# Performance work log

Measured on AMD Instinct MI355X. Metric: run time of the kernel, lower is better.

Reference implementation:

```python
import jax, jax.numpy as jnp
import numpy as np

PARTS_NUM = 16
MAX_INIT = -100.0  # torch scatter_reduce amax include_self initial value


def setup_inputs() -> dict:
    key = jax.random.key(0)
    k1, k2 = jax.random.split(key)
    x = jax.random.normal(k1, (32, 256, 30, 16, 16), dtype=jnp.float32)
    part_labels = jax.random.randint(k2, (32, 30, 16, 16), 0, PARTS_NUM, dtype=jnp.int64)
    return {"x": x, "part_labels": part_labels}


def reference(x, part_labels):
    n, c, s, h, w = x.shape
    ns = n * s
    hw = h * w
    P = PARTS_NUM
    # feat: (ns*hw, c) -- channels-last for efficient segment reductions
    feat = jnp.transpose(x, (0, 2, 3, 4, 1)).reshape(ns * hw, c)
    labels = part_labels.reshape(ns, hw).astype(jnp.int32)
    # one flat segment id per (frame, part) pair
    seg = (labels + jnp.arange(ns, dtype=jnp.int32)[:, None] * P).reshape(ns * hw)
    num_seg = ns * P
    pooled_sum = jax.ops.segment_sum(feat, seg, num_segments=num_seg)          # (ns*P, c)
    pooled_count = jax.ops.segment_sum(jnp.ones((ns * hw,), feat.dtype), seg,
                                       num_segments=num_seg)                   # (ns*P,)
    pooled_max = jax.ops.segment_max(feat, seg, num_segments=num_seg)          # (ns*P, c)
    valid = (pooled_count > 0)[:, None]                                        # (ns*P, 1)
    pooled_mean = pooled_sum / jnp.maximum(pooled_count, 1.0)[:, None]
    # torch scatter_reduce includes initial -100.0 in the amax; empty parts -> 0
    pooled_max = jnp.where(valid, jnp.maximum(pooled_max, MAX_INIT), 0.0)
    pooled = pooled_mean + pooled_max                                          # (ns*P, c)
    # -> (n, c, s, P)
    return jnp.transpose(pooled.reshape(n, s, P, c), (0, 3, 1, 2))
```

## Files before the change

kernel.cpp:

```cpp
#include <hip/hip_runtime.h>


#define C_DIM 256
#define S_DIM 30
#define P_NUM 16
#define HW 256
#define CH_PER_BLK 64
#define TILE_STRIDE 260

__global__ __launch_bounds__(256, 2)
void partpp_pool_kernel(const float* __restrict__ x,
                        const int* __restrict__ labels,
                        float* __restrict__ out) {
    __shared__ float tile[CH_PER_BLK * TILE_STRIDE];
    __shared__ int pos_sorted[HW];
    __shared__ int counts[P_NUM];
    __shared__ int cursor[P_NUM];
    __shared__ int offs[P_NUM + 1];

    const int t  = threadIdx.x;
    const int b  = blockIdx.x;
    const int f  = b >> 2;
    const int q  = b & 3;
    const int ch0 = q * CH_PER_BLK;
    const int n  = f / S_DIM;
    const int s  = f - n * S_DIM;

    if (t < P_NUM) { counts[t] = 0; cursor[t] = 0; }
    __syncthreads();
    const int lab = labels[f * HW + t];
    atomicAdd(&counts[lab], 1);
    __syncthreads();
    if (t == 0) {
        int acc = 0;
        #pragma unroll
        for (int p = 0; p < P_NUM; ++p) { offs[p] = acc; acc += counts[p]; }
        offs[P_NUM] = acc;
    }
    __syncthreads();
    {
        const int r = atomicAdd(&cursor[lab], 1);
        pos_sorted[offs[lab] + r] = t;
    }
    __syncthreads();

    const size_t xbase = ((size_t)(n * C_DIM + ch0) * S_DIM + s) * HW;
    #pragma unroll
    for (int j = 0; j < 16; ++j) {
        const int flat = j * 256 + t;
        const int row  = flat >> 6;
        const int col  = flat & 63;
        const float4 v = *(const float4*)(x + xbase + (size_t)row * (S_DIM * HW) + col * 4);
        *(float4*)(&tile[row * TILE_STRIDE + col * 4]) = v;
    }
    __syncthreads();

    const int ch_l = t >> 2;
    const int sub  = t & 3;
    const float* rowp = &tile[ch_l * TILE_STRIDE];

    float res[4];
    #pragma unroll
    for (int pi = 0; pi < 4; ++pi) {
        const int p  = sub * 4 + pi;
        const int jb = offs[p];
        const int je = offs[p + 1];
        float sum = 0.0f;
        float mx  = -3.0e38f;
        for (int j = jb; j < je; ++j) {
            const float v = rowp[pos_sorted[j]];
            sum += v;
            mx = fmaxf(mx, v);
        }
        const int cnt = je - jb;
        res[pi] = (cnt > 0) ? (sum / (float)cnt + fmaxf(mx, -100.0f)) : 0.0f;
    }

    float* op = out + ((size_t)(n * C_DIM + ch0 + ch_l) * S_DIM + s) * P_NUM + sub * 4;
    *(float4*)op = make_float4(res[0], res[1], res[2], res[3]);
}

extern "C" void kernel_launch(void* const* d_in, const int* in_sizes, int n_in,
                              void* d_out, int out_size, void* d_ws, size_t ws_size,
                              hipStream_t stream) {
    const float* x      = (const float*)d_in[0];
    const int*   labels = (const int*)d_in[1];
    float*       out    = (float*)d_out;

    dim3 grid(960 * 4), block(256);
    hipLaunchKernelGGL(partpp_pool_kernel, grid, block, 0, stream, x, labels, out);
}
```

Before: 341.2 us.

## Scatter tile into label-sorted order, halve channels per block, issue loads early

Global loads of x are now issued into registers before the label counting and prefix-sum phase, so memory latency overlaps with that setup work. Values are scattered into shared memory at their label-sorted rank, which lets the reduction loop read contiguously instead of going through a pos_sorted indirection. Channels per block drop from 64 to 32, doubling the grid and raising the occupancy hint to 4 blocks. The cost is scattered shared-memory writes that may bank-conflict, and twice as many label-processing passes across the grid.

```diff
diff --git a/kernel.cpp b/kernel.cpp
--- a/kernel.cpp
+++ b/kernel.cpp
@@ -5,30 +5,38 @@
 #define S_DIM 30
 #define P_NUM 16
 #define HW 256
-#define CH_PER_BLK 64
-#define TILE_STRIDE 260
+#define CH_PER_BLK 32
+#define TS 260
 
-__global__ __launch_bounds__(256, 2)
+__global__ __launch_bounds__(256, 4)
 void partpp_pool_kernel(const float* __restrict__ x,
                         const int* __restrict__ labels,
                         float* __restrict__ out) {
-    __shared__ float tile[CH_PER_BLK * TILE_STRIDE];
-    __shared__ int pos_sorted[HW];
-    __shared__ int counts[P_NUM];
-    __shared__ int cursor[P_NUM];
-    __shared__ int offs[P_NUM + 1];
+    __shared__ float tile[CH_PER_BLK * TS];
+    __shared__ int rank[HW];
+    __shared__ int counts[P_NUM], cursor[P_NUM], offs[P_NUM + 1];
 
-    const int t  = threadIdx.x;
-    const int b  = blockIdx.x;
-    const int f  = b >> 2;
-    const int q  = b & 3;
+    const int t   = threadIdx.x;
+    const int b   = blockIdx.x;
+    const int f   = b >> 3;
+    const int q   = b & 7;
     const int ch0 = q * CH_PER_BLK;
-    const int n  = f / S_DIM;
-    const int s  = f - n * S_DIM;
+    const int n   = f / S_DIM;
+    const int s   = f - n * S_DIM;
+
+    const int lab = labels[f * HW + t];
+
+    const size_t xbase = ((size_t)(n * C_DIM + ch0) * S_DIM + s) * HW;
+    const int col = t & 63;
+    float4 v[8];
+    #pragma unroll
+    for (int j = 0; j < 8; ++j) {
+        const int row = j * 4 + (t >> 6);
+        v[j] = *(const float4*)(x + xbase + (size_t)row * (S_DIM * HW) + col * 4);
+    }
 
     if (t < P_NUM) { counts[t] = 0; cursor[t] = 0; }
     __syncthreads();
-    const int lab = labels[f * HW + t];
     atomicAdd(&counts[lab], 1);
     __syncthreads();
     if (t == 0) {
@@ -38,46 +46,43 @@
         offs[P_NUM] = acc;
     }
     __syncthreads();
-    {
-        const int r = atomicAdd(&cursor[lab], 1);
-        pos_sorted[offs[lab] + r] = t;
+    rank[t] = offs[lab] + atomicAdd(&cursor[lab], 1);
+    __syncthreads();
+
+    const int4 rk = *(const int4*)&rank[col * 4];
+    #pragma unroll
+    for (int j = 0; j < 8; ++j) {
+        const int row = j * 4 + (t >> 6);
+        float* rp = &tile[row * TS];
+        rp[rk.x] = v[j].x;
+        rp[rk.y] = v[j].y;
+        rp[rk.z] = v[j].z;
+        rp[rk.w] = v[j].w;
     }
     __syncthreads();
 
-    const size_t xbase = ((size_t)(n * C_DIM + ch0) * S_DIM + s) * HW;
+    const int ch  = t >> 3;
+    const int sub = t & 7;
+    const float* rowp = &tile[ch * TS];
+
+    float res[2];
     #pragma unroll
-    for (int j = 0; j < 16; ++j) {
-        const int flat = j * 256 + t;
-        const int row  = flat >> 6;
-        const int col  = flat & 63;
-        const float4 v = *(const float4*)(x + xbase + (size_t)row * (S_DIM * HW) + col * 4);
-        *(float4*)(&tile[row * TILE_STRIDE + col * 4]) = v;
-    }
-    __syncthreads();
-
-    const int ch_l = t >> 2;
-    const int sub  = t & 3;
-    const float* rowp = &tile[ch_l * TILE_STRIDE];
-
-    float res[4];
-    #pragma unroll
-    for (int pi = 0; pi < 4; ++pi) {
-        const int p  = sub * 4 + pi;
+    for (int pi = 0; pi < 2; ++pi) {
+        const int p  = sub * 2 + pi;
         const int jb = offs[p];
         const int je = offs[p + 1];
         float sum = 0.0f;
         float mx  = -3.0e38f;
         for (int j = jb; j < je; ++j) {
-            const float v = rowp[pos_sorted[j]];
-            sum += v;
-            mx = fmaxf(mx, v);
+            const float vv = rowp[j];
+            sum += vv;
+            mx = fmaxf(mx, vv);
         }
-        const int cnt = je - jb;
-        res[pi] = (cnt > 0) ? (sum / (float)cnt + fmaxf(mx, -100.0f)) : 0.0f;
+        res[pi] = (je > jb) ? (sum / (float)(je - jb) + fmaxf(mx, -100.0f)) : 0.0f;
     }
 
-    float* op = out + ((size_t)(n * C_DIM + ch0 + ch_l) * S_DIM + s) * P_NUM + sub * 4;
-    *(float4*)op = make_float4(res[0], res[1], res[2], res[3]);
+    float* op = out + ((size_t)(n * C_DIM + ch0 + ch) * S_DIM + s) * P_NUM + sub * 2;
+    *(float2*)op = make_float2(res[0], res[1]);
 }
 
 extern "C" void kernel_launch(void* const* d_in, const int* in_sizes, int n_in,
@@ -87,6 +92,6 @@
     const int*   labels = (const int*)d_in[1];
     float*       out    = (float*)d_out;
 
-    dim3 grid(960 * 4), block(256);
+    dim3 grid(960 * 8), block(256);
     hipLaunchKernelGGL(partpp_pool_kernel, grid, block, 0, stream, x, labels, out);
 }
```

Result: no change. 336.7 us (-1.3%).
